# Performance work log

Hardware: AMD Instinct MI355X
Metric: run time of the kernel (lower is better)

Reference implementation:

```python
import jax, jax.numpy as jnp
import numpy as np

B, C, H, W = 4, 512, 64, 64
MID = C // 8  # 64


def setup_inputs() -> dict:
    key = jax.random.key(0)
    ks = jax.random.split(key, 8)
    s = 0.02
    return {
        "x": jax.random.normal(ks[0], (B, C, H, W), dtype=jnp.float32),
        "Wq": jax.random.normal(ks[1], (MID, C), dtype=jnp.float32) * s,
        "bq": jax.random.normal(ks[2], (MID,), dtype=jnp.float32) * s,
        "Wk": jax.random.normal(ks[3], (MID, C), dtype=jnp.float32) * s,
        "bk": jax.random.normal(ks[4], (MID,), dtype=jnp.float32) * s,
        "Wv": jax.random.normal(ks[5], (C, C), dtype=jnp.float32) * s,
        "bv": jax.random.normal(ks[6], (C,), dtype=jnp.float32) * s,
        "gamma": jax.random.uniform(ks[7], (1,), dtype=jnp.float32),
    }


def reference(x, Wq, bq, Wk, bk, Wv, bv, gamma):
    b, c, h, w = x.shape
    n = h * w
    xf = x.reshape(b, c, n)  # [B, C, N]
    # 1x1 convs are per-position linear maps
    q = jnp.einsum('mc,bcn->bnm', Wq, xf) + bq            # [B, N, mid]
    k = jnp.einsum('mc,bcn->bmn', Wk, xf) + bk[:, None]   # [B, mid, N]
    sim = jax.nn.softmax(jnp.einsum('bnm,bmj->bnj', q, k), axis=-1)  # [B, N, N]
    v = jnp.einsum('dc,bcn->bdn', Wv, xf) + bv[:, None]   # [B, C, N]
    # feat[:, d, i] = sum_j v[:, d, j] * sim[:, i, j]
    feat = jnp.einsum('bdj,bij->bdi', v, sim)             # [B, C, N]
    out = gamma[0] * feat + xf
    return out.reshape(b, c, h, w)
```

## Files before the change

### kernel.cpp

```cpp
#include <hip/hip_runtime.h>

#define BATCH 4
#define CCH   512
#define NN    4096
#define MIDD  64

typedef unsigned short u16;
typedef unsigned int   u32;
typedef short s8v  __attribute__((ext_vector_type(8)));
typedef float f16v __attribute__((ext_vector_type(16)));

__device__ __forceinline__ u16 f2bf(float f) {
  u32 u = __float_as_uint(f);
  u += 0x7fffu + ((u >> 16) & 1u);
  return (u16)(u >> 16);
}

__device__ __forceinline__ void g2lds16(const u16* g, u16* l) {
  __builtin_amdgcn_global_load_lds(
      (const __attribute__((address_space(1))) u32*)(const void*)g,
      (__attribute__((address_space(3))) u32*)(void*)l, 16, 0, 0);
}

__global__ __launch_bounds__(256) void transpose_cast(
    const float* __restrict__ x, u16* __restrict__ xbT)
{
  const int b  = blockIdx.z;
  const int c0 = blockIdx.y * 64;
  const int n0 = blockIdx.x * 64;
  const int t  = threadIdx.x;
  __shared__ float ts[64 * 65];

  #pragma unroll
  for (int k = 0; k < 4; k++) {
    int idx = t + 256 * k;
    int cc = idx >> 4, n4 = idx & 15;
    float4 v = *(const float4*)&x[((size_t)(b * CCH + c0 + cc)) * NN + n0 + n4 * 4];
    float* p = &ts[cc * 65 + n4 * 4];
    p[0] = v.x; p[1] = v.y; p[2] = v.z; p[3] = v.w;
  }
  __syncthreads();

  const int n = t >> 2, cb = (t & 3) * 16;
  u16 tmp[16];
  #pragma unroll
  for (int j = 0; j < 16; j++) tmp[j] = f2bf(ts[(cb + j) * 65 + n]);
  u16* dst = &xbT[((size_t)b * NN + n0 + n) * CCH + c0 + cb];
  *(uint4*)&dst[0] = *(uint4*)&tmp[0];
  *(uint4*)&dst[8] = *(uint4*)&tmp[8];
}

__global__ __launch_bounds__(256, 2) void proj_gemm(
    const u16* __restrict__ xbT,
    const float* __restrict__ Wq, const float* __restrict__ bq,
    const float* __restrict__ Wk, const float* __restrict__ bk,
    const float* __restrict__ Wv, const float* __restrict__ bv,
    u16* __restrict__ qT, u16* __restrict__ kT, u16* __restrict__ vT)
{
  const int b  = blockIdx.z;
  const int mt = blockIdx.y;
  const int n0 = blockIdx.x * 256;
  const int t  = threadIdx.x;
  const int ln = t & 31, hi = (t & 63) >> 5, w = t >> 6;

  const float* W; const float* bias;
  if (mt < 8)       { W = Wv + (size_t)mt * 64 * CCH; bias = bv + mt * 64; }
  else if (mt == 8) { W = Wq; bias = bq; }
  else              { W = Wk; bias = bk; }

  __shared__ u16 ws[64 * 72];
  __shared__ u16 xs[256 * 72];

  f16v acc[4];
  #pragma unroll
  for (int i = 0; i < 4; i++)
    #pragma unroll
    for (int r = 0; r < 16; r++) acc[i][r] = 0.f;

  for (int c0 = 0; c0 < CCH; c0 += 64) {
    __syncthreads();
    #pragma unroll
    for (int k = 0; k < 4; k++) {
      int idx = t + 256 * k;
      int mm = idx >> 4, c4 = (idx & 15) * 4;
      float4 v = *(const float4*)&W[(size_t)mm * CCH + c0 + c4];
      uint2 p;
      p.x = (u32)f2bf(v.x) | ((u32)f2bf(v.y) << 16);
      p.y = (u32)f2bf(v.z) | ((u32)f2bf(v.w) << 16);
      *(uint2*)&ws[mm * 72 + c4] = p;
    }
    #pragma unroll
    for (int k = 0; k < 8; k++) {
      int idx = t + 256 * k;
      int nn = idx >> 3, c8 = (idx & 7) * 8;
      *(uint4*)&xs[nn * 72 + c8] =
          *(const uint4*)&xbT[((size_t)b * NN + n0 + nn) * CCH + c0 + c8];
    }
    __syncthreads();

    #pragma unroll
    for (int ks = 0; ks < 4; ks++) {
      s8v a0 = *(const s8v*)&ws[(0  + ln) * 72 + hi * 8 + 16 * ks];
      s8v a1 = *(const s8v*)&ws[(32 + ln) * 72 + hi * 8 + 16 * ks];
      s8v b0 = *(const s8v*)&xs[(w * 64 + 0  + ln) * 72 + hi * 8 + 16 * ks];
      s8v b1 = *(const s8v*)&xs[(w * 64 + 32 + ln) * 72 + hi * 8 + 16 * ks];
      acc[0] = __builtin_amdgcn_mfma_f32_32x32x16_bf16(a0, b0, acc[0], 0, 0, 0);
      acc[1] = __builtin_amdgcn_mfma_f32_32x32x16_bf16(a0, b1, acc[1], 0, 0, 0);
      acc[2] = __builtin_amdgcn_mfma_f32_32x32x16_bf16(a1, b0, acc[2], 0, 0, 0);
      acc[3] = __builtin_amdgcn_mfma_f32_32x32x16_bf16(a1, b1, acc[3], 0, 0, 0);
    }
  }

  if (mt < 8) {
    const int m0g = mt * 64;
    #pragma unroll
    for (int mi = 0; mi < 2; mi++)
      #pragma unroll
      for (int ni = 0; ni < 2; ni++) {
        f16v& a = acc[mi * 2 + ni];
        #pragma unroll
        for (int r = 0; r < 16; r++) {
          int row = (r & 3) + 8 * (r >> 2) + 4 * hi;
          int m   = mi * 32 + row;
          float val = a[r] + bias[m];
          vT[((size_t)b * CCH + m0g + m) * NN + n0 + w * 64 + ni * 32 + ln] = f2bf(val);
        }
      }
  } else {
    u16* dst = (mt == 8) ? qT : kT;
    __syncthreads();
    #pragma unroll
    for (int mi = 0; mi < 2; mi++)
      #pragma unroll
      for (int ni = 0; ni < 2; ni++) {
        f16v& a = acc[mi * 2 + ni];
        #pragma unroll
        for (int r = 0; r < 16; r++) {
          int row = (r & 3) + 8 * (r >> 2) + 4 * hi;
          int m   = mi * 32 + row;
          xs[(w * 64 + ni * 32 + ln) * 72 + m] = f2bf(a[r] + bias[m]);
        }
      }
    __syncthreads();
    u16* src = &xs[t * 72];
    u16* drow = &dst[((size_t)b * NN + n0 + t) * 64];
    #pragma unroll
    for (int k = 0; k < 8; k++)
      *(uint4*)&drow[k * 8] = *(uint4*)&src[k * 8];
  }
}

__global__ __launch_bounds__(256, 2) void attn_kernel(
    const u16* __restrict__ qT,
    const u16* __restrict__ kT,
    const u16* __restrict__ vT,
    const float* __restrict__ x,
    const float* __restrict__ gamma,
    float* __restrict__ out)
{
  __shared__ u16 ksm[64 * 64];
  __shared__ u16 plm[64 * 64];
  __shared__ u16 vsm[256 * 64];
  __shared__ float lred[2][64];

  const int bx    = blockIdx.x;
  const int slot  = bx & 7;
  const int b     = slot >> 1;
  const int dbase = (slot & 1) * 256;
  const int i0    = (bx >> 3) * 64;
  const int t     = threadIdx.x;
  const int l     = t & 63, ln = l & 31, hi = l >> 5;
  const int w     = t >> 6;
  const int qh    = w >> 1;
  const int jh    = w & 1;
  const int l3    = l & 7;

  s8v qfrag[4];
  {
    const u16* qp = qT + ((size_t)b * NN + i0 + qh * 32 + ln) * 64 + hi * 8;
    #pragma unroll
    for (int k = 0; k < 4; k++) qfrag[k] = *(const s8v*)(qp + 16 * k);
  }

  const int lh3 = l >> 3;
  const int sw8 = (l3 ^ lh3) * 8;
  const u16* kbase = kT + (size_t)b * NN * 64;
  const u16* vbase = vT + ((size_t)b * CCH + dbase) * NN;
  const u16* ksrc  = kbase + (size_t)(16 * w + lh3) * 64 + sw8;
  const u16* vsrc  = vbase + (size_t)(64 * w + lh3) * NN + sw8;

  f16v oacc[4];
  #pragma unroll
  for (int i = 0; i < 4; i++)
    #pragma unroll
    for (int r = 0; r < 16; r++) oacc[i][r] = 0.f;
  float lpart[16];
  #pragma unroll
  for (int r = 0; r < 16; r++) lpart[r] = 0.f;

  for (int j0 = 0; j0 < NN; j0 += 64) {
    __syncthreads();
    #pragma unroll
    for (int i = 0; i < 2; i++)
      g2lds16(ksrc + (size_t)(j0 + 8 * i) * 64, ksm + (w * 2 + i) * 512);
    #pragma unroll
    for (int i = 0; i < 8; i++)
      g2lds16(vsrc + (size_t)(8 * i) * NN + j0, vsm + (w * 8 + i) * 512);
    __syncthreads();

    f16v sacc;
    #pragma unroll
    for (int r = 0; r < 16; r++) sacc[r] = 0.f;
    #pragma unroll
    for (int ks = 0; ks < 4; ks++) {
      s8v bf = *(const s8v*)&ksm[(jh * 32 + ln) * 64 + (((2 * ks + hi) ^ l3) << 3)];
      sacc = __builtin_amdgcn_mfma_f32_32x32x16_bf16(qfrag[ks], bf, sacc, 0, 0, 0);
    }
    #pragma unroll
    for (int r = 0; r < 16; r++) {
      float p = __expf(sacc[r]);
      lpart[r] += p;
      int row = qh * 32 + (r & 3) + ((r >> 2) << 3) + (hi << 2);
      int r7  = (r & 3) + (hi << 2);
      int jbl = (jh << 2) + (ln >> 3);
      plm[(row << 6) + ((jbl ^ r7) << 3) + (ln & 7)] = f2bf(p);
    }
    __syncthreads();

    #pragma unroll
    for (int ks = 0; ks < 4; ks++) {
      const int cb = ((2 * ks + hi) ^ l3) << 3;
      s8v a0 = *(const s8v*)&plm[(ln << 6) + cb];
      s8v a1 = *(const s8v*)&plm[((32 + ln) << 6) + cb];
      s8v b0 = *(const s8v*)&vsm[(((w << 5) + ln) << 6) + cb];
      s8v b1 = *(const s8v*)&vsm[((((w + 4) << 5) + ln) << 6) + cb];
      oacc[0] = __builtin_amdgcn_mfma_f32_32x32x16_bf16(a0, b0, oacc[0], 0, 0, 0);
      oacc[1] = __builtin_amdgcn_mfma_f32_32x32x16_bf16(a0, b1, oacc[1], 0, 0, 0);
      oacc[2] = __builtin_amdgcn_mfma_f32_32x32x16_bf16(a1, b0, oacc[2], 0, 0, 0);
      oacc[3] = __builtin_amdgcn_mfma_f32_32x32x16_bf16(a1, b1, oacc[3], 0, 0, 0);
    }
  }

  #pragma unroll
  for (int r = 0; r < 16; r++) {
    float v = lpart[r];
    v += __shfl_xor(v, 1);  v += __shfl_xor(v, 2);  v += __shfl_xor(v, 4);
    v += __shfl_xor(v, 8);  v += __shfl_xor(v, 16);
    lpart[r] = v;
  }
  if (ln == 0) {
    #pragma unroll
    for (int r = 0; r < 16; r++) {
      int row = qh * 32 + (r & 3) + ((r >> 2) << 3) + (hi << 2);
      lred[jh][row] = lpart[r];
    }
  }
  __syncthreads();

  const float g0 = gamma[0];
  float* scr = (float*)vsm;
  float* sw_ = scr + w * (32 * 33);
  #pragma unroll
  for (int qt = 0; qt < 2; qt++) {
    const float linv = 1.0f / (lred[0][qt * 32 + ln] + lred[1][qt * 32 + ln]);
    #pragma unroll
    for (int ds = 0; ds < 2; ds++) {
      f16v& a = oacc[qt * 2 + ds];
      __syncthreads();
      #pragma unroll
      for (int r = 0; r < 16; r++)
        sw_[((r & 3) + ((r >> 2) << 3) + (hi << 2)) * 33 + ln] = a[r];
      __syncthreads();
      const int dg = dbase + (w + 4 * ds) * 32;
      #pragma unroll
      for (int r = 0; r < 16; r++) {
        int dl = 2 * r + hi;
        float val = sw_[ln * 33 + dl];
        size_t idx = ((size_t)b * CCH + dg + dl) * NN + i0 + qt * 32 + ln;
        out[idx] = g0 * val * linv + x[idx];
      }
    }
  }
}

extern "C" void kernel_launch(void* const* d_in, const int* in_sizes, int n_in,
                              void* d_out, int out_size, void* d_ws, size_t ws_size,
                              hipStream_t stream) {
  const float* x     = (const float*)d_in[0];
  const float* Wq    = (const float*)d_in[1];
  const float* bq    = (const float*)d_in[2];
  const float* Wk    = (const float*)d_in[3];
  const float* bk    = (const float*)d_in[4];
  const float* Wv    = (const float*)d_in[5];
  const float* bv    = (const float*)d_in[6];
  const float* gamma = (const float*)d_in[7];
  float* out = (float*)d_out;

  u16* qT  = (u16*)d_ws;
  u16* kT  = qT  + (size_t)BATCH * NN * MIDD;
  u16* vT  = kT  + (size_t)BATCH * NN * MIDD;
  u16* xbT = vT  + (size_t)BATCH * CCH * NN;

  transpose_cast<<<dim3(NN / 64, CCH / 64, BATCH), 256, 0, stream>>>(x, xbT);
  proj_gemm<<<dim3(NN / 256, 10, BATCH), 256, 0, stream>>>(
      xbT, Wq, bq, Wk, bk, Wv, bv, qT, kT, vT);
  attn_kernel<<<dim3(512), 256, 0, stream>>>(qT, kT, vT, x, gamma, out);
}
```

Before: 244.9 us.

## Double-buffer K and P tiles in attention loop, swap MFMA operands, async proj loads

The attention loop now double-buffers the K and P tiles in LDS. It prefetches the next K tile while the current one is used, and replaces __syncthreads with raw barriers plus explicit vmcnt waits so loads stay in flight across phases. The PV MFMA operands are swapped so the accumulator layout maps straight to the output, which removes the LDS transpose staging in the epilogue. The projection kernel loads x tiles with global_load_lds into an XOR-swizzled unpadded buffer and reuses that swizzle for the q/k transpose writes. The hand-counted waitcnt values are fragile, and the extra LDS used by the double buffers may lower occupancy.

New measurement: 238.4 us. -2.7%, faster.

```diff
diff --git a/kernel.cpp b/kernel.cpp
--- a/kernel.cpp
+++ b/kernel.cpp
@@ -21,6 +21,9 @@
       (const __attribute__((address_space(1))) u32*)(const void*)g,
       (__attribute__((address_space(3))) u32*)(void*)l, 16, 0, 0);
 }
+
+#define S_WAITCNT(vm, lgkm) \
+  __builtin_amdgcn_s_waitcnt(((vm) & 15) | (((vm) >> 4) << 14) | (0x7 << 4) | ((lgkm) << 8))
 
 __global__ __launch_bounds__(256) void transpose_cast(
     const float* __restrict__ x, u16* __restrict__ xbT)
@@ -62,6 +65,7 @@
   const int n0 = blockIdx.x * 256;
   const int t  = threadIdx.x;
   const int ln = t & 31, hi = (t & 63) >> 5, w = t >> 6;
+  const int l  = t & 63, l3 = l & 7, lh3 = l >> 3;
 
   const float* W; const float* bias;
   if (mt < 8)       { W = Wv + (size_t)mt * 64 * CCH; bias = bv + mt * 64; }
@@ -69,7 +73,9 @@
   else              { W = Wk; bias = bk; }
 
   __shared__ u16 ws[64 * 72];
-  __shared__ u16 xs[256 * 72];
+  __shared__ u16 xs[256 * 64];
+
+  const u16* xsrc = xbT + ((size_t)b * NN + n0 + w * 64 + lh3) * CCH + (l3 ^ lh3) * 8;
 
   f16v acc[4];
   #pragma unroll
@@ -90,20 +96,17 @@
       *(uint2*)&ws[mm * 72 + c4] = p;
     }
     #pragma unroll
-    for (int k = 0; k < 8; k++) {
-      int idx = t + 256 * k;
-      int nn = idx >> 3, c8 = (idx & 7) * 8;
-      *(uint4*)&xs[nn * 72 + c8] =
-          *(const uint4*)&xbT[((size_t)b * NN + n0 + nn) * CCH + c0 + c8];
-    }
+    for (int i = 0; i < 8; i++)
+      g2lds16(xsrc + (size_t)(8 * i) * CCH + c0, xs + (w * 8 + i) * 512);
     __syncthreads();
 
     #pragma unroll
     for (int ks = 0; ks < 4; ks++) {
+      const int cb = ((2 * ks + hi) ^ l3) << 3;
       s8v a0 = *(const s8v*)&ws[(0  + ln) * 72 + hi * 8 + 16 * ks];
       s8v a1 = *(const s8v*)&ws[(32 + ln) * 72 + hi * 8 + 16 * ks];
-      s8v b0 = *(const s8v*)&xs[(w * 64 + 0  + ln) * 72 + hi * 8 + 16 * ks];
-      s8v b1 = *(const s8v*)&xs[(w * 64 + 32 + ln) * 72 + hi * 8 + 16 * ks];
+      s8v b0 = *(const s8v*)&xs[((w * 64 + 0  + ln) << 6) + cb];
+      s8v b1 = *(const s8v*)&xs[((w * 64 + 32 + ln) << 6) + cb];
       acc[0] = __builtin_amdgcn_mfma_f32_32x32x16_bf16(a0, b0, acc[0], 0, 0, 0);
       acc[1] = __builtin_amdgcn_mfma_f32_32x32x16_bf16(a0, b1, acc[1], 0, 0, 0);
       acc[2] = __builtin_amdgcn_mfma_f32_32x32x16_bf16(a1, b0, acc[2], 0, 0, 0);
@@ -129,6 +132,7 @@
   } else {
     u16* dst = (mt == 8) ? qT : kT;
     __syncthreads();
+    u16* xt = (u16*)xs;
     #pragma unroll
     for (int mi = 0; mi < 2; mi++)
       #pragma unroll
@@ -138,15 +142,16 @@
         for (int r = 0; r < 16; r++) {
           int row = (r & 3) + 8 * (r >> 2) + 4 * hi;
           int m   = mi * 32 + row;
-          xs[(w * 64 + ni * 32 + ln) * 72 + m] = f2bf(a[r] + bias[m]);
+          int nr = w * 64 + ni * 32 + ln;
+          xt[(nr << 6) + (((m >> 3) ^ (ln & 7)) << 3) + (m & 7)] = f2bf(a[r] + bias[m]);
         }
       }
     __syncthreads();
-    u16* src = &xs[t * 72];
+    const int r7 = t & 7;
     u16* drow = &dst[((size_t)b * NN + n0 + t) * 64];
     #pragma unroll
     for (int k = 0; k < 8; k++)
-      *(uint4*)&drow[k * 8] = *(uint4*)&src[k * 8];
+      *(uint4*)&drow[k * 8] = *(uint4*)&xt[(t << 6) + ((k ^ r7) << 3)];
   }
 }
 
@@ -158,10 +163,9 @@
     const float* __restrict__ gamma,
     float* __restrict__ out)
 {
-  __shared__ u16 ksm[64 * 64];
-  __shared__ u16 plm[64 * 64];
+  __shared__ u16 ksm[2][64 * 64];
+  __shared__ u16 plm[2][64 * 64];
   __shared__ u16 vsm[256 * 64];
-  __shared__ float lred[2][64];
 
   const int bx    = blockIdx.x;
   const int slot  = bx & 7;
@@ -173,7 +177,8 @@
   const int w     = t >> 6;
   const int qh    = w >> 1;
   const int jh    = w & 1;
-  const int l3    = l & 7;
+  const int l3    = l & 7, lh3 = l >> 3;
+  const int sw8   = (l3 ^ lh3) * 8;
 
   s8v qfrag[4];
   {
@@ -182,8 +187,6 @@
     for (int k = 0; k < 4; k++) qfrag[k] = *(const s8v*)(qp + 16 * k);
   }
 
-  const int lh3 = l >> 3;
-  const int sw8 = (l3 ^ lh3) * 8;
   const u16* kbase = kT + (size_t)b * NN * 64;
   const u16* vbase = vT + ((size_t)b * CCH + dbase) * NN;
   const u16* ksrc  = kbase + (size_t)(16 * w + lh3) * 64 + sw8;
@@ -198,22 +201,32 @@
   #pragma unroll
   for (int r = 0; r < 16; r++) lpart[r] = 0.f;
 
-  for (int j0 = 0; j0 < NN; j0 += 64) {
-    __syncthreads();
-    #pragma unroll
-    for (int i = 0; i < 2; i++)
-      g2lds16(ksrc + (size_t)(j0 + 8 * i) * 64, ksm + (w * 2 + i) * 512);
+  #pragma unroll
+  for (int i = 0; i < 2; i++)
+    g2lds16(ksrc + (size_t)(8 * i) * 64, &ksm[0][(w * 2 + i) * 512]);
+
+  for (int it = 0; it < 64; it++) {
+    const int j0  = it * 64;
+    const int cur = it & 1, nxt = cur ^ 1;
+
+    __builtin_amdgcn_s_barrier();
     #pragma unroll
     for (int i = 0; i < 8; i++)
       g2lds16(vsrc + (size_t)(8 * i) * NN + j0, vsm + (w * 8 + i) * 512);
-    __syncthreads();
+    const int j1 = ((it + 1) & 63) * 64;
+    #pragma unroll
+    for (int i = 0; i < 2; i++)
+      g2lds16(ksrc + (size_t)(j1 + 8 * i) * 64, &ksm[nxt][(w * 2 + i) * 512]);
+
+    S_WAITCNT(10, 15);
+    __builtin_amdgcn_s_barrier();
 
     f16v sacc;
     #pragma unroll
     for (int r = 0; r < 16; r++) sacc[r] = 0.f;
     #pragma unroll
     for (int ks = 0; ks < 4; ks++) {
-      s8v bf = *(const s8v*)&ksm[(jh * 32 + ln) * 64 + (((2 * ks + hi) ^ l3) << 3)];
+      s8v bf = *(const s8v*)&ksm[cur][(jh * 32 + ln) * 64 + (((2 * ks + hi) ^ l3) << 3)];
       sacc = __builtin_amdgcn_mfma_f32_32x32x16_bf16(qfrag[ks], bf, sacc, 0, 0, 0);
     }
     #pragma unroll
@@ -223,24 +236,30 @@
       int row = qh * 32 + (r & 3) + ((r >> 2) << 3) + (hi << 2);
       int r7  = (r & 3) + (hi << 2);
       int jbl = (jh << 2) + (ln >> 3);
-      plm[(row << 6) + ((jbl ^ r7) << 3) + (ln & 7)] = f2bf(p);
-    }
-    __syncthreads();
+      plm[cur][(row << 6) + ((jbl ^ r7) << 3) + (ln & 7)] = f2bf(p);
+    }
+
+    S_WAITCNT(2, 0);
+    __builtin_amdgcn_s_barrier();
 
     #pragma unroll
     for (int ks = 0; ks < 4; ks++) {
       const int cb = ((2 * ks + hi) ^ l3) << 3;
-      s8v a0 = *(const s8v*)&plm[(ln << 6) + cb];
-      s8v a1 = *(const s8v*)&plm[((32 + ln) << 6) + cb];
-      s8v b0 = *(const s8v*)&vsm[(((w << 5) + ln) << 6) + cb];
-      s8v b1 = *(const s8v*)&vsm[((((w + 4) << 5) + ln) << 6) + cb];
-      oacc[0] = __builtin_amdgcn_mfma_f32_32x32x16_bf16(a0, b0, oacc[0], 0, 0, 0);
-      oacc[1] = __builtin_amdgcn_mfma_f32_32x32x16_bf16(a0, b1, oacc[1], 0, 0, 0);
-      oacc[2] = __builtin_amdgcn_mfma_f32_32x32x16_bf16(a1, b0, oacc[2], 0, 0, 0);
-      oacc[3] = __builtin_amdgcn_mfma_f32_32x32x16_bf16(a1, b1, oacc[3], 0, 0, 0);
-    }
-  }
-
+      s8v p0 = *(const s8v*)&plm[cur][(ln << 6) + cb];
+      s8v p1 = *(const s8v*)&plm[cur][((32 + ln) << 6) + cb];
+      s8v v0 = *(const s8v*)&vsm[(((w << 5) + ln) << 6) + cb];
+      s8v v1 = *(const s8v*)&vsm[((((w + 4) << 5) + ln) << 6) + cb];
+      oacc[0] = __builtin_amdgcn_mfma_f32_32x32x16_bf16(v0, p0, oacc[0], 0, 0, 0);
+      oacc[1] = __builtin_amdgcn_mfma_f32_32x32x16_bf16(v0, p1, oacc[1], 0, 0, 0);
+      oacc[2] = __builtin_amdgcn_mfma_f32_32x32x16_bf16(v1, p0, oacc[2], 0, 0, 0);
+      oacc[3] = __builtin_amdgcn_mfma_f32_32x32x16_bf16(v1, p1, oacc[3], 0, 0, 0);
+    }
+  }
+
+  S_WAITCNT(0, 0);
+  __builtin_amdgcn_s_barrier();
+
+  float* lred = (float*)&ksm[0][0];
   #pragma unroll
   for (int r = 0; r < 16; r++) {
     float v = lpart[r];
@@ -252,32 +271,25 @@
     #pragma unroll
     for (int r = 0; r < 16; r++) {
       int row = qh * 32 + (r & 3) + ((r >> 2) << 3) + (hi << 2);
-      lred[jh][row] = lpart[r];
+      lred[jh * 64 + row] = lpart[r];
     }
   }
   __syncthreads();
 
   const float g0 = gamma[0];
-  float* scr = (float*)vsm;
-  float* sw_ = scr + w * (32 * 33);
   #pragma unroll
   for (int qt = 0; qt < 2; qt++) {
-    const float linv = 1.0f / (lred[0][qt * 32 + ln] + lred[1][qt * 32 + ln]);
+    const float linv = 1.0f / (lred[qt * 32 + ln] + lred[64 + qt * 32 + ln]);
+    const int n = i0 + qt * 32 + ln;
     #pragma unroll
     for (int ds = 0; ds < 2; ds++) {
-      f16v& a = oacc[qt * 2 + ds];
-      __syncthreads();
-      #pragma unroll
-      for (int r = 0; r < 16; r++)
-        sw_[((r & 3) + ((r >> 2) << 3) + (hi << 2)) * 33 + ln] = a[r];
-      __syncthreads();
+      f16v& a = oacc[ds * 2 + qt];
       const int dg = dbase + (w + 4 * ds) * 32;
       #pragma unroll
       for (int r = 0; r < 16; r++) {
-        int dl = 2 * r + hi;
-        float val = sw_[ln * 33 + dl];
-        size_t idx = ((size_t)b * CCH + dg + dl) * NN + i0 + qt * 32 + ln;
-        out[idx] = g0 * val * linv + x[idx];
+        int dl = (r & 3) + 8 * (r >> 2) + 4 * hi;
+        size_t idx = ((size_t)b * CCH + dg + dl) * NN + n;
+        out[idx] = g0 * a[r] * linv + x[idx];
       }
     }
   }
```
